# Performance work log

Measured on AMD Instinct MI355X. Metric: run time of the kernel, lower is better.

## Reference

```python
import math
import jax, jax.numpy as jnp
import numpy as np

N_HEAD = 8
BLOCK_SIZE = 1024
LN_EPS = 1e-5


def _layer_norm(x, g, b):
    mu = jnp.mean(x, axis=-1, keepdims=True)
    var = jnp.var(x, axis=-1, keepdims=True)
    return (x - mu) * jax.lax.rsqrt(var + LN_EPS) * g + b


def _skew(QEr):
    # QEr: (B, nh, L, L) -> pad one zero column on the left, reshape, drop first row
    B, nh, nr, nc = QEr.shape
    padded = jnp.pad(QEr, ((0, 0), (0, 0), (0, 0), (1, 0)))  # (B, nh, nr, nc+1)
    reshaped = padded.reshape(B, nh, nc + 1, nr)
    return reshaped[:, :, 1:, :]  # (B, nh, nr, nc)


def _attn(x, W_qkv, b_qkv, W_o, b_o, Er):
    B, L, D = x.shape
    hs = D // N_HEAD
    qkv = x @ W_qkv + b_qkv  # (B, L, 3D)
    q, k, v = jnp.split(qkv, 3, axis=-1)
    # (B, nh, L, hs)
    q = q.reshape(B, L, N_HEAD, hs).transpose(0, 2, 1, 3)
    k = k.reshape(B, L, N_HEAD, hs).transpose(0, 2, 1, 3)
    v = v.reshape(B, L, N_HEAD, hs).transpose(0, 2, 1, 3)
    start = BLOCK_SIZE - L
    Er_t = Er[start:, :].T  # (hs, L)
    QEr = q @ Er_t  # (B, nh, L, L)
    Srel = _skew(QEr)
    scores = (jnp.einsum('bhqd,bhkd->bhqk', q, k) + Srel) * (1.0 / math.sqrt(hs))
    causal = jnp.tril(jnp.ones((L, L), dtype=bool))
    scores = jnp.where(causal, scores, jnp.float32(-jnp.inf))
    att = jax.nn.softmax(scores, axis=-1)
    y = jnp.einsum('bhqk,bhkd->bhqd', att, v)
    y = y.transpose(0, 2, 1, 3).reshape(B, L, D)
    return y @ W_o + b_o


def reference(x, W_qkv, b_qkv, W_o, b_o, Er, ln1_g, ln1_b, ln2_g, ln2_b,
              W_fc, b_fc, W_proj, b_proj):
    x = x + _attn(_layer_norm(x, ln1_g, ln1_b), W_qkv, b_qkv, W_o, b_o, Er)
    h = _layer_norm(x, ln2_g, ln2_b) @ W_fc + b_fc
    h = jax.nn.gelu(h, approximate=False)
    h = h @ W_proj + b_proj
    return x + h


def setup_inputs() -> dict:
    key = jax.random.key(0)
    ks = jax.random.split(key, 8)
    B, L, D, F = 8, 1024, 1024, 4096
    hs = D // N_HEAD
    s = lambda fan_in: 1.0 / math.sqrt(fan_in)
    return {
        'x': jax.random.normal(ks[0], (B, L, D), dtype=jnp.float32),
        'W_qkv': jax.random.normal(ks[1], (D, 3 * D), dtype=jnp.float32) * s(D),
        'b_qkv': jnp.zeros((3 * D,), dtype=jnp.float32),
        'W_o': jax.random.normal(ks[2], (D, D), dtype=jnp.float32) * s(D),
        'b_o': jnp.zeros((D,), dtype=jnp.float32),
        'Er': jax.random.normal(ks[3], (BLOCK_SIZE, hs), dtype=jnp.float32),
        'ln1_g': jnp.ones((D,), dtype=jnp.float32),
        'ln1_b': jnp.zeros((D,), dtype=jnp.float32),
        'ln2_g': jnp.ones((D,), dtype=jnp.float32),
        'ln2_b': jnp.zeros((D,), dtype=jnp.float32),
        'W_fc': jax.random.normal(ks[4], (D, F), dtype=jnp.float32) * s(D),
        'b_fc': jnp.zeros((F,), dtype=jnp.float32),
        'W_proj': jax.random.normal(ks[5], (F, D), dtype=jnp.float32) * s(F),
        'b_proj': jnp.zeros((D,), dtype=jnp.float32),
    }
```

## Files before the change

### kernel.cpp

```cpp
#include <hip/hip_runtime.h>
#include <hip/hip_bf16.h>
#include <math.h>

#define BB 8
#define LL 1024
#define DD 1024
#define FF 4096
#define NHH 8
#define HSS 128
#define SCALE 0.08838834764831845f
#define TRI(qi, kt) ((qi) * ((qi) + 1) / 2 + (kt))

typedef __bf16 bf16;
typedef __bf16 bf16x8 __attribute__((ext_vector_type(8)));
typedef float f32x4 __attribute__((ext_vector_type(4)));
typedef _Float16 f16;
typedef _Float16 f16x4 __attribute__((ext_vector_type(4)));

__device__ inline void async_copy16(const void* g, void* l) {
  __builtin_amdgcn_global_load_lds(
      (const __attribute__((address_space(1))) unsigned int*)g,
      (__attribute__((address_space(3))) unsigned int*)l, 16, 0, 0);
}

__global__ __launch_bounds__(256)
void transpose_cast_kernel(const float* __restrict__ W, bf16* __restrict__ Wt,
                           int K, int N) {
  __shared__ float tile[32][33];
  int n0 = blockIdx.x * 32, k0 = blockIdx.y * 32;
  int tx = threadIdx.x, ty = threadIdx.y;
#pragma unroll
  for (int i = 0; i < 32; i += 8)
    tile[ty + i][tx] = W[(size_t)(k0 + ty + i) * N + n0 + tx];
  __syncthreads();
#pragma unroll
  for (int i = 0; i < 32; i += 8)
    Wt[(size_t)(n0 + ty + i) * K + k0 + tx] = (bf16)tile[tx][ty + i];
}

__global__ __launch_bounds__(256)
void cast_bf16_kernel(const float* __restrict__ src, bf16* __restrict__ dst, int n) {
  int i = blockIdx.x * blockDim.x + threadIdx.x;
  if (i < n) dst[i] = (bf16)src[i];
}

__global__ __launch_bounds__(256)
void ln_kernel(const float* __restrict__ x, const float* __restrict__ g,
               const float* __restrict__ bta, bf16* __restrict__ out) {
  int row = blockIdx.x;
  int tid = threadIdx.x;
  const float4 v = ((const float4*)(x + (size_t)row * DD))[tid];
  float s = v.x + v.y + v.z + v.w;
  float s2 = v.x * v.x + v.y * v.y + v.z * v.z + v.w * v.w;
#pragma unroll
  for (int o = 32; o > 0; o >>= 1) {
    s += __shfl_down(s, o);
    s2 += __shfl_down(s2, o);
  }
  __shared__ float a1[4], a2[4];
  int wave = tid >> 6;
  if ((tid & 63) == 0) { a1[wave] = s; a2[wave] = s2; }
  __syncthreads();
  s = a1[0] + a1[1] + a1[2] + a1[3];
  s2 = a2[0] + a2[1] + a2[2] + a2[3];
  float mu = s * (1.0f / DD);
  float rstd = rsqrtf(s2 * (1.0f / DD) - mu * mu + 1e-5f);
  float4 gv = ((const float4*)g)[tid];
  float4 bv = ((const float4*)bta)[tid];
  bf16* o4 = out + (size_t)row * DD + tid * 4;
  o4[0] = (bf16)((v.x - mu) * rstd * gv.x + bv.x);
  o4[1] = (bf16)((v.y - mu) * rstd * gv.y + bv.y);
  o4[2] = (bf16)((v.z - mu) * rstd * gv.z + bv.z);
  o4[3] = (bf16)((v.w - mu) * rstd * gv.w + bv.w);
}

template <int EPI>
__global__ __launch_bounds__(256)
void gemm_kernel(const bf16* __restrict__ A, const bf16* __restrict__ Bt,
                 const float* __restrict__ bias, const float* __restrict__ res,
                 void* __restrict__ Cout, int M, int N, int K) {
  __shared__ bf16 Als[128 * 32];
  __shared__ bf16 Bls[128 * 32];
  int tid = threadIdx.x;
  int wave = tid >> 6, lane = tid & 63;
  int l15 = lane & 15, quad = lane >> 4;
  int m0 = blockIdx.y * 128, n0 = blockIdx.x * 128;
  int wm = (wave >> 1) * 64, wn = (wave & 1) * 64;
  f32x4 acc[4][4] = {};

  for (int k0 = 0; k0 < K; k0 += 32) {
    __syncthreads();
#pragma unroll
    for (int i = 0; i < 2; i++) {
      int t = i * 256 + tid;
      int row = t >> 2, kc = (t & 3) << 3;
      async_copy16(A + (size_t)(m0 + row) * K + k0 + kc, &Als[t * 8]);
      async_copy16(Bt + (size_t)(n0 + row) * K + k0 + kc, &Bls[t * 8]);
    }
    __syncthreads();
    bf16x8 af[4], bfr[4];
#pragma unroll
    for (int mt = 0; mt < 4; mt++)
      af[mt] = *(const bf16x8*)&Als[(wm + mt * 16 + l15) * 32 + quad * 8];
#pragma unroll
    for (int nt = 0; nt < 4; nt++)
      bfr[nt] = *(const bf16x8*)&Bls[(wn + nt * 16 + l15) * 32 + quad * 8];
#pragma unroll
    for (int mt = 0; mt < 4; mt++)
#pragma unroll
      for (int nt = 0; nt < 4; nt++)
        acc[mt][nt] = __builtin_amdgcn_mfma_f32_16x16x32_bf16(af[mt], bfr[nt],
                                                              acc[mt][nt], 0, 0, 0);
  }

#pragma unroll
  for (int mt = 0; mt < 4; mt++) {
#pragma unroll
    for (int nt = 0; nt < 4; nt++) {
      int col = n0 + wn + nt * 16 + l15;
      float bv = bias[col];
#pragma unroll
      for (int r = 0; r < 4; r++) {
        int row = m0 + wm + mt * 16 + quad * 4 + r;
        float v = acc[mt][nt][r] + bv;
        if (EPI == 1) v = 0.5f * v * (1.0f + erff(v * 0.7071067811865475f));
        if (EPI == 2) {
          v += res[(size_t)row * N + col];
          ((float*)Cout)[(size_t)row * N + col] = v;
        } else {
          ((bf16*)Cout)[(size_t)row * N + col] = (bf16)v;
        }
      }
    }
  }
}

__global__ __launch_bounds__(256)
void pack_kv_kernel(const bf16* __restrict__ qkv, bf16* __restrict__ Kpack,
                    bf16* __restrict__ Vpack) {
  __shared__ bf16 Vst[64][132];
  int kt = blockIdx.x, h = blockIdx.y, b = blockIdx.z;
  int tid = threadIdx.x;
  const size_t rs = 3 * DD;
  const bf16* kb = qkv + (size_t)b * LL * rs + (size_t)(kt * 64) * rs + DD + h * HSS;
  const bf16* vb = kb + DD;
  bf16* kp = Kpack + ((size_t)(b * NHH + h) * 16 + kt) * (64 * 128);
  bf16* vp = Vpack + ((size_t)(b * NHH + h) * 16 + kt) * (128 * 64);
#pragma unroll
  for (int i = 0; i < 4; i++) {
    int u = i * 256 + tid;
    int kk = u >> 4, c = u & 15;
    bf16x8 kv = *(const bf16x8*)(kb + (size_t)kk * rs + c * 8);
    *(bf16x8*)(kp + kk * 128 + ((c ^ kk) & 15) * 8) = kv;
    *(bf16x8*)&Vst[kk][c * 8] = *(const bf16x8*)(vb + (size_t)kk * rs + c * 8);
  }
  __syncthreads();
#pragma unroll
  for (int i = 0; i < 4; i++) {
    int u = i * 256 + tid;
    int d = u >> 3, c = u & 7;
    bf16x8 t;
#pragma unroll
    for (int j = 0; j < 8; j++) t[j] = Vst[c * 8 + j][d];
    *(bf16x8*)(vp + d * 64 + ((c ^ (d & 7))) * 8) = t;
  }
}

__global__ __launch_bounds__(256)
void relband_kernel(const bf16* __restrict__ qkv, const bf16* __restrict__ Erb,
                    f16* __restrict__ band) {
  int t = blockIdx.x;
  int h = blockIdx.y, b = blockIdx.z;
  int qi = (int)((sqrtf((float)(8 * t + 1)) - 1.0f) * 0.5f);
  while (TRI(qi + 1, 0) <= t) qi++;
  while (TRI(qi, 0) > t) qi--;
  int kt = t - TRI(qi, 0);

  int tid = threadIdx.x, wave = tid >> 6, lane = tid & 63;
  int l15 = lane & 15, quad = lane >> 4;
  int qw0 = qi * 64 + wave * 16;
  int k0 = kt * 64;
  const size_t rs = 3 * DD;
  const bf16* qbase = qkv + (size_t)b * LL * rs + h * HSS;
  bf16x8 qf[4];
#pragma unroll
  for (int st = 0; st < 4; st++)
    qf[st] = *(const bf16x8*)(qbase + (size_t)(qw0 + l15) * rs + st * 32 + quad * 8);

  int kmax_off = qw0 + 15 - k0;
  int m_base = 1008 - qw0 + k0;
  int ntR = (kmax_off >> 4) + 1;
  if (ntR > 4) ntR = 4;
  f32x4 rr[5] = {};
#pragma unroll
  for (int n = 0; n < 5; n++) {
    if (n <= ntR) {
      int mr = m_base + n * 16 + l15;
      mr = mr < 0 ? 0 : (mr > 1023 ? 1023 : mr);
#pragma unroll
      for (int st = 0; st < 4; st++) {
        bf16x8 ef = *(const bf16x8*)(Erb + (size_t)mr * HSS + st * 32 + quad * 8);
        rr[n] = __builtin_amdgcn_mfma_f32_16x16x32_bf16(qf[st], ef, rr[n], 0, 0, 0);
      }
    }
  }
  f16x4 sf[4];
#pragma unroll
  for (int rg = 0; rg < 4; rg++) {
    int qloc = quad * 4 + rg;
    int tt = 15 - qloc + l15;
    int src = (lane & 48) | (tt & 15);
    float shv[5];
#pragma unroll
    for (int n = 0; n < 5; n++)
      shv[n] = (n <= ntR) ? __shfl(rr[n][rg], src) : 0.f;
#pragma unroll
    for (int nt = 0; nt < 4; nt++)
      sf[nt][rg] = (f16)((tt & 16) ? shv[nt + 1] : shv[nt]);
  }
  f16* tb = band + (size_t)(b * NHH + h) * (136 * 4096) + (size_t)t * 4096;
#pragma unroll
  for (int nt = 0; nt < 4; nt++)
    if (nt * 16 <= kmax_off)
      *(f16x4*)(tb + (wave * 4 + nt) * 256 + l15 * 16 + quad * 4) = sf[nt];
}

__global__ __launch_bounds__(256)
void flash_kernel(const bf16* __restrict__ qkv, const bf16* __restrict__ Kpack,
                  const bf16* __restrict__ Vpack, const f16* __restrict__ band,
                  bf16* __restrict__ y) {
  __shared__ bf16 Kls[64 * 128];
  __shared__ bf16 Vls[128 * 64];
  __shared__ bf16 Pls[4][16][72];

  int tid = threadIdx.x, wave = tid >> 6, lane = tid & 63;
  int l15 = lane & 15, quad = lane >> 4;
  int qb = 15 - blockIdx.x;
  int h = blockIdx.y, b = blockIdx.z;
  int qw0 = qb * 64 + wave * 16;

  const size_t rs = 3 * DD;
  const bf16* qbase = qkv + (size_t)b * LL * rs + h * HSS;
  const bf16* kp = Kpack + (size_t)(b * NHH + h) * 16 * (64 * 128);
  const bf16* vp = Vpack + (size_t)(b * NHH + h) * 16 * (128 * 64);
  const f16* bnd = band + (size_t)(b * NHH + h) * (136 * 4096);

  bf16x8 qf[4];
#pragma unroll
  for (int st = 0; st < 4; st++)
    qf[st] = *(const bf16x8*)(qbase + (size_t)(qw0 + l15) * rs + st * 32 + quad * 8);

  f32x4 o[8] = {};
  float mrow[4] = {-INFINITY, -INFINITY, -INFINITY, -INFINITY};
  float lrow[4] = {0.f, 0.f, 0.f, 0.f};

  int nkt = qb + 1;
  for (int kt = 0; kt < nkt; kt++) {
    int k0 = kt * 64;
    int kmax_off = qw0 + 15 - k0;
    __syncthreads();
    {
      const bf16* ks = kp + (size_t)kt * (64 * 128);
      const bf16* vs = vp + (size_t)kt * (128 * 64);
#pragma unroll
      for (int i = 0; i < 4; i++) {
        int off = (wave * 4 + i) * 512 + lane * 8;
        async_copy16(ks + off, &Kls[off]);
        async_copy16(vs + off, &Vls[off]);
      }
    }
    const f16* tb = bnd + (size_t)TRI(qb, kt) * 4096;
    f16x4 srl[4] = {};
#pragma unroll
    for (int nt = 0; nt < 4; nt++)
      if (nt * 16 <= kmax_off)
        srl[nt] = *(const f16x4*)(tb + (wave * 4 + nt) * 256 + l15 * 16 + quad * 4);
    __syncthreads();

    f32x4 sa[4] = {};
#pragma unroll
    for (int nt = 0; nt < 4; nt++) {
      if (nt * 16 <= kmax_off) {
        int kk = nt * 16 + l15;
#pragma unroll
        for (int st = 0; st < 4; st++) {
          bf16x8 kf = *(const bf16x8*)&Kls[kk * 128 + (((st * 4 + quad) ^ l15) & 15) * 8];
          sa[nt] = __builtin_amdgcn_mfma_f32_16x16x32_bf16(qf[st], kf, sa[nt], 0, 0, 0);
        }
      }
    }

    float pmx[4] = {-INFINITY, -INFINITY, -INFINITY, -INFINITY};
#pragma unroll
    for (int nt = 0; nt < 4; nt++) {
      if (nt * 16 <= kmax_off) {
        int kg = k0 + nt * 16 + l15;
#pragma unroll
        for (int rg = 0; rg < 4; rg++) {
          int qg = qw0 + quad * 4 + rg;
          float v = (sa[nt][rg] + (float)srl[nt][rg]) * SCALE;
          v = (kg <= qg) ? v : -INFINITY;
          sa[nt][rg] = v;
          pmx[rg] = fmaxf(pmx[rg], v);
        }
      } else {
#pragma unroll
        for (int rg = 0; rg < 4; rg++) sa[nt][rg] = -INFINITY;
      }
    }

#pragma unroll
    for (int rg = 0; rg < 4; rg++) {
      float v = pmx[rg];
      v = fmaxf(v, __shfl_xor(v, 1));
      v = fmaxf(v, __shfl_xor(v, 2));
      v = fmaxf(v, __shfl_xor(v, 4));
      v = fmaxf(v, __shfl_xor(v, 8));
      float mnew = fmaxf(mrow[rg], v);
      float alpha = __expf(mrow[rg] - mnew);
      mrow[rg] = mnew;
      lrow[rg] *= alpha;
#pragma unroll
      for (int nt = 0; nt < 8; nt++) o[nt][rg] *= alpha;
      pmx[rg] = mnew;
    }
    float ls[4] = {0.f, 0.f, 0.f, 0.f};
#pragma unroll
    for (int nt = 0; nt < 4; nt++)
#pragma unroll
      for (int rg = 0; rg < 4; rg++) {
        float p = __expf(sa[nt][rg] - pmx[rg]);
        ls[rg] += p;
        Pls[wave][quad * 4 + rg][nt * 16 + l15] = (bf16)p;
      }
#pragma unroll
    for (int rg = 0; rg < 4; rg++) {
      float v = ls[rg];
      v += __shfl_xor(v, 1);
      v += __shfl_xor(v, 2);
      v += __shfl_xor(v, 4);
      v += __shfl_xor(v, 8);
      lrow[rg] += v;
    }

    bf16x8 pf[2];
#pragma unroll
    for (int s2 = 0; s2 < 2; s2++)
      pf[s2] = *(const bf16x8*)&Pls[wave][l15][s2 * 32 + quad * 8];
#pragma unroll
    for (int nt = 0; nt < 8; nt++) {
      int d = nt * 16 + l15;
#pragma unroll
      for (int s2 = 0; s2 < 2; s2++) {
        if (s2 * 32 <= kmax_off) {
          bf16x8 vf = *(const bf16x8*)&Vls[d * 64 + (((s2 * 4 + quad) ^ (l15 & 7)) & 7) * 8];
          o[nt] = __builtin_amdgcn_mfma_f32_16x16x32_bf16(pf[s2], vf, o[nt], 0, 0, 0);
        }
      }
    }
  }

#pragma unroll
  for (int rg = 0; rg < 4; rg++) {
    float inv = 1.0f / lrow[rg];
    int qg = qw0 + quad * 4 + rg;
    bf16* yr = y + ((size_t)b * LL + qg) * DD + h * HSS;
#pragma unroll
    for (int nt = 0; nt < 8; nt++) yr[nt * 16 + l15] = (bf16)(o[nt][rg] * inv);
  }
}

extern "C" void kernel_launch(void* const* d_in, const int* in_sizes, int n_in,
                              void* d_out, int out_size, void* d_ws, size_t ws_size,
                              hipStream_t stream) {
  const float* x = (const float*)d_in[0];
  const float* W_qkv = (const float*)d_in[1];
  const float* b_qkv = (const float*)d_in[2];
  const float* W_o = (const float*)d_in[3];
  const float* b_o = (const float*)d_in[4];
  const float* Er = (const float*)d_in[5];
  const float* ln1_g = (const float*)d_in[6];
  const float* ln1_b = (const float*)d_in[7];
  const float* ln2_g = (const float*)d_in[8];
  const float* ln2_b = (const float*)d_in[9];
  const float* W_fc = (const float*)d_in[10];
  const float* b_fc = (const float*)d_in[11];
  const float* W_proj = (const float*)d_in[12];
  const float* b_proj = (const float*)d_in[13];
  float* out = (float*)d_out;

  char* p = (char*)d_ws;
  auto alloc = [&](size_t bytes) {
    char* r = p;
    p += (bytes + 255) & ~(size_t)255;
    return r;
  };
  bf16* Wt_qkv = (bf16*)alloc((size_t)3072 * 1024 * 2);
  bf16* Wt_o   = (bf16*)alloc((size_t)1024 * 1024 * 2);
  bf16* Wt_fc  = (bf16*)alloc((size_t)4096 * 1024 * 2);
  bf16* Wt_pr  = (bf16*)alloc((size_t)1024 * 4096 * 2);
  bf16* Erb    = (bf16*)alloc((size_t)1024 * 128 * 2);
  bf16* xn     = (bf16*)alloc((size_t)8192 * 1024 * 2);
  bf16* qkvb   = (bf16*)alloc((size_t)8192 * 3072 * 2);
  bf16* yb     = (bf16*)alloc((size_t)8192 * 1024 * 2);
  bf16* Kpack  = (bf16*)alloc((size_t)64 * 16 * 64 * 128 * 2);
  bf16* Vpack  = (bf16*)alloc((size_t)64 * 16 * 128 * 64 * 2);
  f16*  band   = (f16*)alloc((size_t)64 * 136 * 4096 * 2);
  float* x2    = (float*)band;
  bf16* hb     = qkvb;

  transpose_cast_kernel<<<dim3(3072 / 32, 1024 / 32), dim3(32, 8), 0, stream>>>(W_qkv, Wt_qkv, 1024, 3072);
  transpose_cast_kernel<<<dim3(1024 / 32, 1024 / 32), dim3(32, 8), 0, stream>>>(W_o, Wt_o, 1024, 1024);
  transpose_cast_kernel<<<dim3(4096 / 32, 1024 / 32), dim3(32, 8), 0, stream>>>(W_fc, Wt_fc, 1024, 4096);
  transpose_cast_kernel<<<dim3(1024 / 32, 4096 / 32), dim3(32, 8), 0, stream>>>(W_proj, Wt_pr, 4096, 1024);
  cast_bf16_kernel<<<512, 256, 0, stream>>>(Er, Erb, 1024 * 128);

  ln_kernel<<<8192, 256, 0, stream>>>(x, ln1_g, ln1_b, xn);
  gemm_kernel<0><<<dim3(24, 64), 256, 0, stream>>>(xn, Wt_qkv, b_qkv, nullptr, qkvb, 8192, 3072, 1024);
  pack_kv_kernel<<<dim3(16, 8, 8), 256, 0, stream>>>(qkvb, Kpack, Vpack);
  relband_kernel<<<dim3(136, 8, 8), 256, 0, stream>>>(qkvb, Erb, band);
  flash_kernel<<<dim3(16, 8, 8), 256, 0, stream>>>(qkvb, Kpack, Vpack, band, yb);
  gemm_kernel<2><<<dim3(8, 64), 256, 0, stream>>>(yb, Wt_o, b_o, x, x2, 8192, 1024, 1024);
  ln_kernel<<<8192, 256, 0, stream>>>(x2, ln2_g, ln2_b, xn);
  gemm_kernel<1><<<dim3(32, 64), 256, 0, stream>>>(xn, Wt_fc, b_fc, nullptr, hb, 8192, 4096, 1024);
  gemm_kernel<2><<<dim3(8, 64), 256, 0, stream>>>(hb, Wt_pr, b_proj, x2, out, 8192, 1024, 4096);
}
```

Baseline: 730.3 us.

## Double-buffer K/V tiles and pair causal query blocks per workgroup in flash attention

The flash attention kernel now double-buffers the K and V shared-memory tiles. The next tile's async global-to-LDS copy is issued before computing on the current one, so load latency overlaps with MFMA work. Each workgroup also processes two query blocks, qb and 15-qb, in sequence, and the grid is halved. This evens out the triangular causal workload across blocks. The cost is twice the LDS for K/V, which may limit how many blocks fit on a CU, and a longer serial run per workgroup.

After: 691.0 us. -5.4%, faster.

```diff
diff --git a/kernel.cpp b/kernel.cpp
--- a/kernel.cpp
+++ b/kernel.cpp
@@ -229,15 +229,13 @@
 void flash_kernel(const bf16* __restrict__ qkv, const bf16* __restrict__ Kpack,
                   const bf16* __restrict__ Vpack, const f16* __restrict__ band,
                   bf16* __restrict__ y) {
-  __shared__ bf16 Kls[64 * 128];
-  __shared__ bf16 Vls[128 * 64];
+  __shared__ bf16 Kls[2][64 * 128];
+  __shared__ bf16 Vls[2][128 * 64];
   __shared__ bf16 Pls[4][16][72];
 
   int tid = threadIdx.x, wave = tid >> 6, lane = tid & 63;
   int l15 = lane & 15, quad = lane >> 4;
-  int qb = 15 - blockIdx.x;
   int h = blockIdx.y, b = blockIdx.z;
-  int qw0 = qb * 64 + wave * 16;
 
   const size_t rs = 3 * DD;
   const bf16* qbase = qkv + (size_t)b * LL * rs + h * HSS;
@@ -245,128 +243,149 @@
   const bf16* vp = Vpack + (size_t)(b * NHH + h) * 16 * (128 * 64);
   const f16* bnd = band + (size_t)(b * NHH + h) * (136 * 4096);
 
-  bf16x8 qf[4];
-#pragma unroll
-  for (int st = 0; st < 4; st++)
-    qf[st] = *(const bf16x8*)(qbase + (size_t)(qw0 + l15) * rs + st * 32 + quad * 8);
-
-  f32x4 o[8] = {};
-  float mrow[4] = {-INFINITY, -INFINITY, -INFINITY, -INFINITY};
-  float lrow[4] = {0.f, 0.f, 0.f, 0.f};
-
-  int nkt = qb + 1;
-  for (int kt = 0; kt < nkt; kt++) {
-    int k0 = kt * 64;
-    int kmax_off = qw0 + 15 - k0;
-    __syncthreads();
+  int buf = 0;
+#pragma unroll 1
+  for (int ph = 0; ph < 2; ph++) {
+    int qb = ph ? 15 - blockIdx.x : blockIdx.x;
+    int qw0 = qb * 64 + wave * 16;
+    int nkt = qb + 1;
+
+    bf16x8 qf[4];
+#pragma unroll
+    for (int st = 0; st < 4; st++)
+      qf[st] = *(const bf16x8*)(qbase + (size_t)(qw0 + l15) * rs + st * 32 + quad * 8);
+
     {
-      const bf16* ks = kp + (size_t)kt * (64 * 128);
-      const bf16* vs = vp + (size_t)kt * (128 * 64);
+      const bf16* ks = kp;
+      const bf16* vs = vp;
 #pragma unroll
       for (int i = 0; i < 4; i++) {
         int off = (wave * 4 + i) * 512 + lane * 8;
-        async_copy16(ks + off, &Kls[off]);
-        async_copy16(vs + off, &Vls[off]);
-      }
-    }
-    const f16* tb = bnd + (size_t)TRI(qb, kt) * 4096;
-    f16x4 srl[4] = {};
-#pragma unroll
-    for (int nt = 0; nt < 4; nt++)
-      if (nt * 16 <= kmax_off)
-        srl[nt] = *(const f16x4*)(tb + (wave * 4 + nt) * 256 + l15 * 16 + quad * 4);
-    __syncthreads();
-
-    f32x4 sa[4] = {};
-#pragma unroll
-    for (int nt = 0; nt < 4; nt++) {
-      if (nt * 16 <= kmax_off) {
-        int kk = nt * 16 + l15;
-#pragma unroll
-        for (int st = 0; st < 4; st++) {
-          bf16x8 kf = *(const bf16x8*)&Kls[kk * 128 + (((st * 4 + quad) ^ l15) & 15) * 8];
-          sa[nt] = __builtin_amdgcn_mfma_f32_16x16x32_bf16(qf[st], kf, sa[nt], 0, 0, 0);
-        }
-      }
-    }
-
-    float pmx[4] = {-INFINITY, -INFINITY, -INFINITY, -INFINITY};
-#pragma unroll
-    for (int nt = 0; nt < 4; nt++) {
-      if (nt * 16 <= kmax_off) {
-        int kg = k0 + nt * 16 + l15;
+        async_copy16(ks + off, &Kls[buf][off]);
+        async_copy16(vs + off, &Vls[buf][off]);
+      }
+    }
+
+    f32x4 o[8] = {};
+    float mrow[4] = {-INFINITY, -INFINITY, -INFINITY, -INFINITY};
+    float lrow[4] = {0.f, 0.f, 0.f, 0.f};
+
+#pragma unroll 1
+    for (int kt = 0; kt < nkt; kt++) {
+      int k0 = kt * 64;
+      int kmax_off = qw0 + 15 - k0;
+      __syncthreads();
+
+      const f16* tb = bnd + (size_t)TRI(qb, kt) * 4096;
+      f16x4 srl[4] = {};
+#pragma unroll
+      for (int nt = 0; nt < 4; nt++)
+        if (nt * 16 <= kmax_off)
+          srl[nt] = *(const f16x4*)(tb + (wave * 4 + nt) * 256 + l15 * 16 + quad * 4);
+
+      if (kt + 1 < nkt) {
+        const bf16* ks = kp + (size_t)(kt + 1) * (64 * 128);
+        const bf16* vs = vp + (size_t)(kt + 1) * (128 * 64);
+#pragma unroll
+        for (int i = 0; i < 4; i++) {
+          int off = (wave * 4 + i) * 512 + lane * 8;
+          async_copy16(ks + off, &Kls[buf ^ 1][off]);
+          async_copy16(vs + off, &Vls[buf ^ 1][off]);
+        }
+      }
+
+      f32x4 sa[4] = {};
+#pragma unroll
+      for (int nt = 0; nt < 4; nt++) {
+        if (nt * 16 <= kmax_off) {
+          int kk = nt * 16 + l15;
+#pragma unroll
+          for (int st = 0; st < 4; st++) {
+            bf16x8 kf = *(const bf16x8*)&Kls[buf][kk * 128 + (((st * 4 + quad) ^ l15) & 15) * 8];
+            sa[nt] = __builtin_amdgcn_mfma_f32_16x16x32_bf16(qf[st], kf, sa[nt], 0, 0, 0);
+          }
+        }
+      }
+
+      float pmx[4] = {-INFINITY, -INFINITY, -INFINITY, -INFINITY};
+#pragma unroll
+      for (int nt = 0; nt < 4; nt++) {
+        if (nt * 16 <= kmax_off) {
+          int kg = k0 + nt * 16 + l15;
+#pragma unroll
+          for (int rg = 0; rg < 4; rg++) {
+            int qg = qw0 + quad * 4 + rg;
+            float v = (sa[nt][rg] + (float)srl[nt][rg]) * SCALE;
+            v = (kg <= qg) ? v : -INFINITY;
+            sa[nt][rg] = v;
+            pmx[rg] = fmaxf(pmx[rg], v);
+          }
+        } else {
+#pragma unroll
+          for (int rg = 0; rg < 4; rg++) sa[nt][rg] = -INFINITY;
+        }
+      }
+
+#pragma unroll
+      for (int rg = 0; rg < 4; rg++) {
+        float v = pmx[rg];
+        v = fmaxf(v, __shfl_xor(v, 1));
+        v = fmaxf(v, __shfl_xor(v, 2));
+        v = fmaxf(v, __shfl_xor(v, 4));
+        v = fmaxf(v, __shfl_xor(v, 8));
+        float mnew = fmaxf(mrow[rg], v);
+        float alpha = __expf(mrow[rg] - mnew);
+        mrow[rg] = mnew;
+        lrow[rg] *= alpha;
+#pragma unroll
+        for (int nt = 0; nt < 8; nt++) o[nt][rg] *= alpha;
+        pmx[rg] = mnew;
+      }
+      float ls[4] = {0.f, 0.f, 0.f, 0.f};
+#pragma unroll
+      for (int nt = 0; nt < 4; nt++)
 #pragma unroll
         for (int rg = 0; rg < 4; rg++) {
-          int qg = qw0 + quad * 4 + rg;
-          float v = (sa[nt][rg] + (float)srl[nt][rg]) * SCALE;
-          v = (kg <= qg) ? v : -INFINITY;
-          sa[nt][rg] = v;
-          pmx[rg] = fmaxf(pmx[rg], v);
-        }
-      } else {
-#pragma unroll
-        for (int rg = 0; rg < 4; rg++) sa[nt][rg] = -INFINITY;
-      }
+          float p = __expf(sa[nt][rg] - pmx[rg]);
+          ls[rg] += p;
+          Pls[wave][quad * 4 + rg][nt * 16 + l15] = (bf16)p;
+        }
+#pragma unroll
+      for (int rg = 0; rg < 4; rg++) {
+        float v = ls[rg];
+        v += __shfl_xor(v, 1);
+        v += __shfl_xor(v, 2);
+        v += __shfl_xor(v, 4);
+        v += __shfl_xor(v, 8);
+        lrow[rg] += v;
+      }
+
+      bf16x8 pf[2];
+#pragma unroll
+      for (int s2 = 0; s2 < 2; s2++)
+        pf[s2] = *(const bf16x8*)&Pls[wave][l15][s2 * 32 + quad * 8];
+#pragma unroll
+      for (int nt = 0; nt < 8; nt++) {
+        int d = nt * 16 + l15;
+#pragma unroll
+        for (int s2 = 0; s2 < 2; s2++) {
+          if (s2 * 32 <= kmax_off) {
+            bf16x8 vf = *(const bf16x8*)&Vls[buf][d * 64 + (((s2 * 4 + quad) ^ (l15 & 7)) & 7) * 8];
+            o[nt] = __builtin_amdgcn_mfma_f32_16x16x32_bf16(pf[s2], vf, o[nt], 0, 0, 0);
+          }
+        }
+      }
+      buf ^= 1;
     }
 
 #pragma unroll
     for (int rg = 0; rg < 4; rg++) {
-      float v = pmx[rg];
-      v = fmaxf(v, __shfl_xor(v, 1));
-      v = fmaxf(v, __shfl_xor(v, 2));
-      v = fmaxf(v, __shfl_xor(v, 4));
-      v = fmaxf(v, __shfl_xor(v, 8));
-      float mnew = fmaxf(mrow[rg], v);
-      float alpha = __expf(mrow[rg] - mnew);
-      mrow[rg] = mnew;
-      lrow[rg] *= alpha;
-#pragma unroll
-      for (int nt = 0; nt < 8; nt++) o[nt][rg] *= alpha;
-      pmx[rg] = mnew;
-    }
-    float ls[4] = {0.f, 0.f, 0.f, 0.f};
-#pragma unroll
-    for (int nt = 0; nt < 4; nt++)
-#pragma unroll
-      for (int rg = 0; rg < 4; rg++) {
-        float p = __expf(sa[nt][rg] - pmx[rg]);
-        ls[rg] += p;
-        Pls[wave][quad * 4 + rg][nt * 16 + l15] = (bf16)p;
-      }
-#pragma unroll
-    for (int rg = 0; rg < 4; rg++) {
-      float v = ls[rg];
-      v += __shfl_xor(v, 1);
-      v += __shfl_xor(v, 2);
-      v += __shfl_xor(v, 4);
-      v += __shfl_xor(v, 8);
-      lrow[rg] += v;
-    }
-
-    bf16x8 pf[2];
-#pragma unroll
-    for (int s2 = 0; s2 < 2; s2++)
-      pf[s2] = *(const bf16x8*)&Pls[wave][l15][s2 * 32 + quad * 8];
-#pragma unroll
-    for (int nt = 0; nt < 8; nt++) {
-      int d = nt * 16 + l15;
-#pragma unroll
-      for (int s2 = 0; s2 < 2; s2++) {
-        if (s2 * 32 <= kmax_off) {
-          bf16x8 vf = *(const bf16x8*)&Vls[d * 64 + (((s2 * 4 + quad) ^ (l15 & 7)) & 7) * 8];
-          o[nt] = __builtin_amdgcn_mfma_f32_16x16x32_bf16(pf[s2], vf, o[nt], 0, 0, 0);
-        }
-      }
-    }
-  }
-
-#pragma unroll
-  for (int rg = 0; rg < 4; rg++) {
-    float inv = 1.0f / lrow[rg];
-    int qg = qw0 + quad * 4 + rg;
-    bf16* yr = y + ((size_t)b * LL + qg) * DD + h * HSS;
-#pragma unroll
-    for (int nt = 0; nt < 8; nt++) yr[nt * 16 + l15] = (bf16)(o[nt][rg] * inv);
+      float inv = 1.0f / lrow[rg];
+      int qg = qw0 + quad * 4 + rg;
+      bf16* yr = y + ((size_t)b * LL + qg) * DD + h * HSS;
+#pragma unroll
+      for (int nt = 0; nt < 8; nt++) yr[nt * 16 + l15] = (bf16)(o[nt][rg] * inv);
+    }
   }
 }
 
@@ -419,7 +438,7 @@
   gemm_kernel<0><<<dim3(24, 64), 256, 0, stream>>>(xn, Wt_qkv, b_qkv, nullptr, qkvb, 8192, 3072, 1024);
   pack_kv_kernel<<<dim3(16, 8, 8), 256, 0, stream>>>(qkvb, Kpack, Vpack);
   relband_kernel<<<dim3(136, 8, 8), 256, 0, stream>>>(qkvb, Erb, band);
-  flash_kernel<<<dim3(16, 8, 8), 256, 0, stream>>>(qkvb, Kpack, Vpack, band, yb);
+  flash_kernel<<<dim3(8, 8, 8), 256, 0, stream>>>(qkvb, Kpack, Vpack, band, yb);
   gemm_kernel<2><<<dim3(8, 64), 256, 0, stream>>>(yb, Wt_o, b_o, x, x2, 8192, 1024, 1024);
   ln_kernel<<<8192, 256, 0, stream>>>(x2, ln2_g, ln2_b, xn);
   gemm_kernel<1><<<dim3(32, 64), 256, 0, stream>>>(xn, Wt_fc, b_fc, nullptr, hb, 8192, 4096, 1024);
```
